# Performance work log

Measured on AMD Instinct MI355X. Metric: run time of the kernel, lower is better.

## Reference

```python
import jax, jax.numpy as jnp
import numpy as np

S = 1024      # sequence length
V = 32000     # vocab size
H = 1024      # hidden_dim
A = 128       # attn_size (module default)


def lstm_cell(x, h, c, Wih, Whh, b):
    # torch LSTM gate order: i, f, g, o
    g = x @ Wih.T + h @ Whh.T + b
    i, f, gg, o = jnp.split(g, 4)
    c = jax.nn.sigmoid(f) * c + jax.nn.sigmoid(i) * jnp.tanh(gg)
    h = jax.nn.sigmoid(o) * jnp.tanh(c)
    return h, c


def setup_inputs() -> dict:
    key = jax.random.key(0)
    ks = jax.random.split(key, 16)
    p = lambda k, shape: (jax.random.normal(k, shape, jnp.float32) * 0.02)
    return {
        'input_seq': jax.random.randint(ks[0], (S,), 0, V),
        'gold_seq': jax.random.randint(ks[1], (S,), 0, V),
        'embed': p(ks[2], (V, H)),
        'enc_Wih': p(ks[3], (4 * H, H)),
        'enc_Whh': p(ks[4], (4 * H, H)),
        'enc_b': jnp.zeros((4 * H,), jnp.float32),   # b_ih + b_hh combined
        'dec_Wih': p(ks[5], (4 * H, 2 * H)),          # decoder input = [prev, context]
        'dec_Whh': p(ks[6], (4 * H, H)),
        'dec_b': jnp.zeros((4 * H,), jnp.float32),
        'U_w': p(ks[7], (A, H)), 'U_b': jnp.zeros((A,), jnp.float32),
        'Wa_w': p(ks[8], (A, H)), 'Wa_b': jnp.zeros((A,), jnp.float32),
        'Va_w': p(ks[9], (1, A)), 'Va_b': jnp.zeros((1,), jnp.float32),
        'out_w': p(ks[10], (V, H)), 'out_b': jnp.zeros((V,), jnp.float32),
    }


def reference(input_seq, gold_seq, embed, enc_Wih, enc_Whh, enc_b,
              dec_Wih, dec_Whh, dec_b, U_w, U_b, Wa_w, Wa_b, Va_w, Va_b,
              out_w, out_b):
    Hd = embed.shape[1]
    x_emb = embed[input_seq]  # (S, H)

    def enc_step(carry, x):
        h, c = carry
        h, c = lstm_cell(x, h, c, enc_Wih, enc_Whh, enc_b)
        return (h, c), h

    zero = jnp.zeros((Hd,), x_emb.dtype)
    (h0, c0), enc_out = jax.lax.scan(enc_step, (zero, zero), x_emb)  # enc_out: (S, H)

    U_enc = enc_out @ U_w.T + U_b  # (S, A), hidden-independent part of additive attention

    # teacher forcing: prev_0 = zeros, prev_i = embed(gold[i-1]); relu applied each step
    prev = jnp.concatenate([jnp.zeros((1, Hd), x_emb.dtype), embed[gold_seq[:-1]]], axis=0)
    prev = jax.nn.relu(prev)  # (S, H)

    def dec_step(carry, p):
        h, c = carry
        # additive attention scores: V(tanh(U(enc) + W(h)))  -> (S, 1)
        scores = jnp.tanh(U_enc + h @ Wa_w.T + Wa_b) @ Va_w.T + Va_b
        # faithful to nn.Softmax() on a (S,1) tensor: torch picks dim=1 -> all ones
        w = jax.nn.softmax(scores, axis=1)  # (S, 1), == ones
        context = w[:, 0] @ enc_out         # (H,) == sum of encoder outputs
        x = jnp.concatenate([p, context])   # (2H,)
        h, c = lstm_cell(x, h, c, dec_Wih, dec_Whh, dec_b)
        logits = h @ out_w.T + out_b        # (V,)
        return (h, c), (logits, jnp.argmax(logits))

    _, (preds, idxs) = jax.lax.scan(dec_step, (h0, c0), prev)
    return preds, idxs  # (S, V) float logits, (S,) predicted ids
```

## Files before the change

### kernel.cpp

```cpp
#include <hip/hip_runtime.h>
#include <math.h>


#define S_LEN 1024
#define HDIM  1024
#define VDIM  32000

typedef float f4 __attribute__((ext_vector_type(4)));
typedef float f32x4 __attribute__((ext_vector_type(4)));
typedef short short8 __attribute__((ext_vector_type(8)));
typedef short sh4 __attribute__((ext_vector_type(4)));

__device__ __forceinline__ void agent_storef(float* p, float v) {
    __hip_atomic_store(p, v, __ATOMIC_RELAXED, __HIP_MEMORY_SCOPE_AGENT);
}
__device__ __forceinline__ float sigmoidf_(float x) {
    return 1.0f / (1.0f + expf(-x));
}
__device__ __forceinline__ void llc_load_4x4(const float* p, f4& a, f4& b,
                                             f4& c, f4& d) {
    asm volatile(
        "global_load_dwordx4 %0, %4, off sc0 sc1\n\t"
        "global_load_dwordx4 %1, %4, off offset:1024 sc0 sc1\n\t"
        "global_load_dwordx4 %2, %4, off offset:2048 sc0 sc1\n\t"
        "global_load_dwordx4 %3, %4, off offset:3072 sc0 sc1\n\t"
        "s_waitcnt vmcnt(0)"
        : "=&v"(a), "=&v"(b), "=&v"(c), "=&v"(d)
        : "v"(p) : "memory");
}
__device__ __forceinline__ bool any_nan16(f4 a, f4 b, f4 c, f4 d) {
    float s0 = (a.x + a.y) + (a.z + a.w);
    float s1 = (b.x + b.y) + (b.z + b.w);
    float s2 = (c.x + c.y) + (c.z + c.w);
    float s3 = (d.x + d.y) + (d.z + d.w);
    float s  = (s0 + s1) + (s2 + s3);
    return s != s;
}
__device__ __forceinline__ int swz(int s) {
    return (s & ~7) | ((s ^ (s >> 3)) & 7);
}
__device__ __forceinline__ void split_bf16(float x, unsigned short& h,
                                           unsigned short& l) {
    unsigned u = __float_as_uint(x);
    unsigned hr = (u + 0x7FFFu + ((u >> 16) & 1u)) >> 16;
    h = (unsigned short)hr;
    float hf = __uint_as_float(hr << 16);
    float r = x - hf;
    unsigned v = __float_as_uint(r);
    l = (unsigned short)((v + 0x7FFFu + ((v >> 16) & 1u)) >> 16);
}

template<int MODE>
__global__ __launch_bounds__(256)
void gemm_nt(const float* __restrict__ B, int ldb,
             const float* __restrict__ bias,
             float* __restrict__ C, int ldc,
             const float* __restrict__ embed,
             const int* __restrict__ gidx,
             int M, int N, int K)
{
    __shared__ float As[16][128];
    __shared__ float Bs[16][128];

    const int tid = threadIdx.x;
    const int m0 = blockIdx.y * 128;
    const int n0 = blockIdx.x * 128;

    float acc[8][8];
#pragma unroll
    for (int r = 0; r < 8; ++r)
#pragma unroll
        for (int c = 0; c < 8; ++c) acc[r][c] = 0.0f;

    const int ty = tid >> 4;
    const int tx = tid & 15;

    for (int k0 = 0; k0 < K; k0 += 16) {
#pragma unroll
        for (int q = 0; q < 2; ++q) {
            int id = tid * 2 + q;
            int m  = id >> 2;
            int c4 = (id & 3) * 4;
            float4 v;
            if (MODE == 1) {
                int row = gidx[m0 + m];
                v = *(const float4*)(embed + (size_t)row * HDIM + k0 + c4);
            } else {
                int mg = m0 + m;
                if (mg == 0) {
                    v = make_float4(0.f, 0.f, 0.f, 0.f);
                } else {
                    int row = gidx[mg - 1];
                    v = *(const float4*)(embed + (size_t)row * HDIM + k0 + c4);
                    v.x = fmaxf(v.x, 0.f); v.y = fmaxf(v.y, 0.f);
                    v.z = fmaxf(v.z, 0.f); v.w = fmaxf(v.w, 0.f);
                }
            }
            As[c4 + 0][m] = v.x; As[c4 + 1][m] = v.y;
            As[c4 + 2][m] = v.z; As[c4 + 3][m] = v.w;
        }
#pragma unroll
        for (int q = 0; q < 2; ++q) {
            int id = tid * 2 + q;
            int n  = id >> 2;
            int c4 = (id & 3) * 4;
            float4 v = *(const float4*)(B + (size_t)(n0 + n) * ldb + k0 + c4);
            Bs[c4 + 0][n] = v.x; Bs[c4 + 1][n] = v.y;
            Bs[c4 + 2][n] = v.z; Bs[c4 + 3][n] = v.w;
        }
        __syncthreads();

#pragma unroll
        for (int k = 0; k < 16; ++k) {
            float4 a0 = *(const float4*)&As[k][ty * 8];
            float4 a1 = *(const float4*)&As[k][ty * 8 + 4];
            float4 b0 = *(const float4*)&Bs[k][tx * 8];
            float4 b1 = *(const float4*)&Bs[k][tx * 8 + 4];
            float av[8] = {a0.x,a0.y,a0.z,a0.w,a1.x,a1.y,a1.z,a1.w};
            float bv[8] = {b0.x,b0.y,b0.z,b0.w,b1.x,b1.y,b1.z,b1.w};
#pragma unroll
            for (int r = 0; r < 8; ++r)
#pragma unroll
                for (int c = 0; c < 8; ++c)
                    acc[r][c] = fmaf(av[r], bv[c], acc[r][c]);
        }
        __syncthreads();
    }

    const int mbase = m0 + ty * 8;
    const int nbase = n0 + tx * 8;
#pragma unroll
    for (int r = 0; r < 8; ++r) {
        float4 o0, o1;
        o0.x = acc[r][0] + bias[nbase + 0];
        o0.y = acc[r][1] + bias[nbase + 1];
        o0.z = acc[r][2] + bias[nbase + 2];
        o0.w = acc[r][3] + bias[nbase + 3];
        o1.x = acc[r][4] + bias[nbase + 4];
        o1.y = acc[r][5] + bias[nbase + 5];
        o1.z = acc[r][6] + bias[nbase + 6];
        o1.w = acc[r][7] + bias[nbase + 7];
        *(float4*)(C + (size_t)(mbase + r) * ldc + nbase)     = o0;
        *(float4*)(C + (size_t)(mbase + r) * ldc + nbase + 4) = o1;
    }
}

__global__ __launch_bounds__(512, 2)
void lstm_seq(const float* __restrict__ Whh,
              const float* __restrict__ G,
              const float* __restrict__ h_init,
              const float* __restrict__ c_init,
              float* __restrict__ h_out,
              float* __restrict__ c_fin,
              float* __restrict__ csum_out,
              int slen)
{
    __shared__ f4 hbuf[256];
    const int tid = threadIdx.x;
    const int g   = blockIdx.x;
    const int wv  = tid >> 6;
    const int lg  = tid & 63;
    const int j   = g * 8 + wv;

    f4 W[4][4];
#pragma unroll
    for (int q = 0; q < 4; ++q)
#pragma unroll
        for (int i = 0; i < 4; ++i)
            W[q][i] = *(const f4*)(Whh + (size_t)(j + q * HDIM) * HDIM
                                   + 4 * lg + 256 * i);

    float c = 0.0f, csum = 0.0f;
    if (lg == 0) c = c_init[j];

    float gnow = G[(size_t)(lg & 3) * HDIM + j];

    for (int t = 0; t < slen; ++t) {
#pragma unroll
        for (int q = 0; q < 4; ++q)
#pragma unroll
            for (int i = 0; i < 4; ++i)
                asm volatile("" : "+v"(W[q][i]));

        const float* hp = (t == 0) ? h_init : (h_out + (size_t)(t - 1) * HDIM);

        if (wv == 0) {
            f4 a, b, cc, d;
            const float* p = hp + 4 * lg;
            for (;;) {
                llc_load_4x4(p, a, b, cc, d);
                if (!__any(any_nan16(a, b, cc, d))) break;
                __builtin_amdgcn_s_sleep(1);
            }
            hbuf[swz(lg)]       = a;
            hbuf[swz(64 + lg)]  = b;
            hbuf[swz(128 + lg)] = cc;
            hbuf[swz(192 + lg)] = d;
        }
        __syncthreads();

        int tn = (t + 1 < slen) ? (t + 1) : t;
        float gnext = G[(size_t)tn * (4 * HDIM) + (lg & 3) * HDIM + j];

        f4 h0 = hbuf[swz(lg)];
        f4 h1 = hbuf[swz(64 + lg)];
        f4 h2 = hbuf[swz(128 + lg)];
        f4 h3 = hbuf[swz(192 + lg)];
        float p0 = 0.f, p1 = 0.f, p2 = 0.f, p3 = 0.f;
        f4 hv;
#pragma unroll
        for (int i = 0; i < 4; ++i) {
            hv = (i == 0) ? h0 : (i == 1) ? h1 : (i == 2) ? h2 : h3;
            p0 = fmaf(W[0][i].x, hv.x, fmaf(W[0][i].y, hv.y,
                 fmaf(W[0][i].z, hv.z, fmaf(W[0][i].w, hv.w, p0))));
            p1 = fmaf(W[1][i].x, hv.x, fmaf(W[1][i].y, hv.y,
                 fmaf(W[1][i].z, hv.z, fmaf(W[1][i].w, hv.w, p1))));
            p2 = fmaf(W[2][i].x, hv.x, fmaf(W[2][i].y, hv.y,
                 fmaf(W[2][i].z, hv.z, fmaf(W[2][i].w, hv.w, p2))));
            p3 = fmaf(W[3][i].x, hv.x, fmaf(W[3][i].y, hv.y,
                 fmaf(W[3][i].z, hv.z, fmaf(W[3][i].w, hv.w, p3))));
        }

        float t01 = __shfl_xor((lg & 1) ? p0 : p1, 1);
        float s01 = ((lg & 1) ? p1 : p0) + t01;
        float t23 = __shfl_xor((lg & 1) ? p2 : p3, 1);
        float s23 = ((lg & 1) ? p3 : p2) + t23;
        float tq  = __shfl_xor((lg & 2) ? s01 : s23, 2);
        float s   = ((lg & 2) ? s23 : s01) + tq;
        s += __shfl_xor(s, 4);
        s += __shfl_xor(s, 8);
        s += __shfl_xor(s, 16);
        s += __shfl_xor(s, 32);

        float pre = s + gnow;
        float act = ((lg & 3) == 2) ? tanhf(pre) : sigmoidf_(pre);
        float a1 = __shfl(act, 1);
        float a2 = __shfl(act, 2);
        float a3 = __shfl(act, 3);

        if (lg == 0) {
            c = a1 * c + act * a2;
            float h = a3 * tanhf(c);
            csum += h;
            agent_storef(h_out + (size_t)t * HDIM + j, h);
        }
        gnow = gnext;
        __syncthreads();
    }

    if (lg == 0) {
        if (c_fin)    c_fin[j]    = c;
        if (csum_out) csum_out[j] = csum;
    }
}

__global__ __launch_bounds__(256)
void ctx_bias_k(const float* __restrict__ dec_Wih,
                const float* __restrict__ dec_b,
                const float* __restrict__ ctx,
                float* __restrict__ out)
{
    const int wv = threadIdx.x >> 6;
    const int lane = threadIdx.x & 63;
    const int r = blockIdx.x * 4 + wv;
    const float* wr = dec_Wih + (size_t)r * (2 * HDIM) + HDIM;
    float s = 0.f;
    for (int k = lane; k < HDIM; k += 64) s += wr[k] * ctx[k];
#pragma unroll
    for (int off = 32; off > 0; off >>= 1) s += __shfl_xor(s, off);
    if (lane == 0) out[r] = s + dec_b[r];
}

#define LSTR 40

__global__ __launch_bounds__(512, 1)
void logits_mfma(const float* __restrict__ Amat,
                 const float* __restrict__ Bmat,
                 const float* __restrict__ bias,
                 float* __restrict__ C,
                 unsigned long long* __restrict__ amax)
{
    __shared__ unsigned short Ah[256][LSTR], Al[256][LSTR];
    __shared__ unsigned short Bh[128][LSTR], Bl[128][LSTR];

    const int tid = threadIdx.x;
    const int l   = tid & 63;
    const int w   = tid >> 6;
    const int n0  = blockIdx.x * 128;
    const int m0  = blockIdx.y * 256;
    const int mb  = (w >> 1) * 64;
    const int nb  = (w & 1) * 64;

    f32x4 acc[4][4];
#pragma unroll
    for (int i = 0; i < 4; ++i)
#pragma unroll
        for (int jj = 0; jj < 4; ++jj) acc[i][jj] = (f32x4){0.f, 0.f, 0.f, 0.f};

    for (int k0 = 0; k0 < HDIM; k0 += 32) {
#pragma unroll
        for (int q = 0; q < 4; ++q) {
            int id  = q * 512 + tid;
            int row = id >> 3;
            int kq  = (id & 7) * 4;
            float4 av = *(const float4*)(Amat + (size_t)(m0 + row) * HDIM
                                         + k0 + kq);
            unsigned short h0,h1,h2,h3, l0,l1,l2,l3;
            split_bf16(av.x, h0, l0); split_bf16(av.y, h1, l1);
            split_bf16(av.z, h2, l2); split_bf16(av.w, h3, l3);
            sh4 hi = {(short)h0, (short)h1, (short)h2, (short)h3};
            sh4 lo = {(short)l0, (short)l1, (short)l2, (short)l3};
            *(sh4*)&Ah[row][kq] = hi;
            *(sh4*)&Al[row][kq] = lo;
        }
#pragma unroll
        for (int q = 0; q < 2; ++q) {
            int id  = q * 512 + tid;
            int row = id >> 3;
            int kq  = (id & 7) * 4;
            float4 bv = *(const float4*)(Bmat + (size_t)(n0 + row) * HDIM
                                         + k0 + kq);
            unsigned short h0,h1,h2,h3, l0,l1,l2,l3;
            split_bf16(bv.x, h0, l0); split_bf16(bv.y, h1, l1);
            split_bf16(bv.z, h2, l2); split_bf16(bv.w, h3, l3);
            sh4 hi = {(short)h0, (short)h1, (short)h2, (short)h3};
            sh4 lo = {(short)l0, (short)l1, (short)l2, (short)l3};
            *(sh4*)&Bh[row][kq] = hi;
            *(sh4*)&Bl[row][kq] = lo;
        }
        __syncthreads();

        const int kb = (l >> 4) * 8;
        short8 a_hi[4], a_lo[4], b_hi[4], b_lo[4];
#pragma unroll
        for (int i = 0; i < 4; ++i) {
            int ra = mb + i * 16 + (l & 15);
            int rb = nb + i * 16 + (l & 15);
            a_hi[i] = *(const short8*)&Ah[ra][kb];
            a_lo[i] = *(const short8*)&Al[ra][kb];
            b_hi[i] = *(const short8*)&Bh[rb][kb];
            b_lo[i] = *(const short8*)&Bl[rb][kb];
        }
#pragma unroll
        for (int i = 0; i < 4; ++i)
#pragma unroll
            for (int jj = 0; jj < 4; ++jj) {
                acc[i][jj] = __builtin_amdgcn_mfma_f32_16x16x32_bf16(
                    a_hi[i], b_hi[jj], acc[i][jj], 0, 0, 0);
                acc[i][jj] = __builtin_amdgcn_mfma_f32_16x16x32_bf16(
                    a_hi[i], b_lo[jj], acc[i][jj], 0, 0, 0);
                acc[i][jj] = __builtin_amdgcn_mfma_f32_16x16x32_bf16(
                    a_lo[i], b_hi[jj], acc[i][jj], 0, 0, 0);
            }
        __syncthreads();
    }

#pragma unroll
    for (int i = 0; i < 4; ++i) {
        const int mrow = m0 + mb + i * 16 + ((l >> 4) << 2);
        unsigned long long key[4] = {0ull, 0ull, 0ull, 0ull};
#pragma unroll
        for (int jj = 0; jj < 4; ++jj) {
            int n = n0 + nb + jj * 16 + (l & 15);
            float bv = bias[n];
            f32x4 o = acc[i][jj];
#pragma unroll
            for (int r = 0; r < 4; ++r) {
                float val = o[r] + bv;
                C[(size_t)(mrow + r) * VDIM + n] = val;
                unsigned um = __float_as_uint(val);
                um = (um & 0x80000000u) ? ~um : (um | 0x80000000u);
                unsigned long long k2 = ((unsigned long long)um << 32)
                    | (unsigned long long)(0xFFFFFFFFu - (unsigned)n);
                if (k2 > key[r]) key[r] = k2;
            }
        }
#pragma unroll
        for (int r = 0; r < 4; ++r) {
#pragma unroll
            for (int off = 1; off < 16; off <<= 1) {
                unsigned long long other = __shfl_xor(key[r], off);
                if (other > key[r]) key[r] = other;
            }
            if ((l & 15) == 0)
                atomicMax(&amax[mrow + r], key[r]);
        }
    }
}

__global__ __launch_bounds__(256)
void idx_final(const unsigned long long* __restrict__ amax,
               float* __restrict__ out_idx)
{
    int i = blockIdx.x * 256 + threadIdx.x;
    if (i < S_LEN) {
        unsigned col = 0xFFFFFFFFu - (unsigned)(amax[i] & 0xFFFFFFFFull);
        out_idx[i] = (float)col;
    }
}

extern "C" void kernel_launch(void* const* d_in, const int* in_sizes, int n_in,
                              void* d_out, int out_size, void* d_ws, size_t ws_size,
                              hipStream_t stream)
{
    (void)in_sizes; (void)n_in; (void)out_size; (void)ws_size;

    const int*   input_seq = (const int*)d_in[0];
    const int*   gold_seq  = (const int*)d_in[1];
    const float* embed     = (const float*)d_in[2];
    const float* enc_Wih   = (const float*)d_in[3];
    const float* enc_Whh   = (const float*)d_in[4];
    const float* enc_b     = (const float*)d_in[5];
    const float* dec_Wih   = (const float*)d_in[6];
    const float* dec_Whh   = (const float*)d_in[7];
    const float* dec_b     = (const float*)d_in[8];
    const float* out_w     = (const float*)d_in[15];
    const float* out_b     = (const float*)d_in[16];

    float* out = (float*)d_out;
    float* G_enc = out;
    float* G_dec = out + 4194304;

    char* wsb = (char*)d_ws;
    unsigned long long* amax = (unsigned long long*)wsb;
    float* zerovec = (float*)(wsb + 8192);
    float* c0      = zerovec + 1024;
    float* ctx     = c0 + 1024;
    float* ctxb    = ctx + 1024;
    float* enc_out = ctxb + 4096;
    float* dec_h   = enc_out + 1048576;

    hipMemsetAsync(d_ws, 0, 12288, stream);
    hipMemsetAsync(enc_out, 0xFF, (size_t)S_LEN * HDIM * 4, stream);
    hipMemsetAsync(dec_h,   0xFF, (size_t)S_LEN * HDIM * 4, stream);

    gemm_nt<1><<<dim3(32, 8), 256, 0, stream>>>(
        enc_Wih, HDIM, enc_b, G_enc, 4 * HDIM,
        embed, input_seq, S_LEN, 4 * HDIM, HDIM);

    lstm_seq<<<128, 512, 0, stream>>>(
        enc_Whh, G_enc, zerovec, zerovec, enc_out, c0, ctx, S_LEN);

    ctx_bias_k<<<1024, 256, 0, stream>>>(dec_Wih, dec_b, ctx, ctxb);

    gemm_nt<2><<<dim3(32, 8), 256, 0, stream>>>(
        dec_Wih, 2 * HDIM, ctxb, G_dec, 4 * HDIM,
        embed, gold_seq, S_LEN, 4 * HDIM, HDIM);

    lstm_seq<<<128, 512, 0, stream>>>(
        dec_Whh, G_dec, enc_out + (size_t)(S_LEN - 1) * HDIM, c0,
        dec_h, nullptr, nullptr, S_LEN);

    logits_mfma<<<dim3(VDIM / 128, S_LEN / 256), 512, 0, stream>>>(
        dec_h, out_w, out_b, out, amax);

    idx_final<<<4, 256, 0, stream>>>(amax, out + (size_t)S_LEN * VDIM);
}
```

Before: 4.715 ms.

## Use split-bf16 MFMA for gate projection GEMMs and double-buffer LSTM h broadcast

Replaces the scalar FP32 tiled GEMM for the encoder and decoder input-gate projections with an MFMA kernel. It splits fp32 operands into hi/lo bf16 parts and accumulates three products to keep near-fp32 accuracy. The LSTM recurrence kernel also double-buffers its shared h buffer by timestep parity, which lets it drop the trailing per-step __syncthreads. The GEMMs are a small share of runtime next to the two sequential 1024-step LSTMs. Removing the barrier could shave latency from every recurrent step, but only if the parity buffers are truly race-free.

Result: faster. 4.372 ms (-7.3%).

```diff
diff --git a/kernel.cpp b/kernel.cpp
--- a/kernel.cpp
+++ b/kernel.cpp
@@ -50,98 +50,121 @@
     l = (unsigned short)((v + 0x7FFFu + ((v >> 16) & 1u)) >> 16);
 }
 
+#define LSTR 40
+
 template<int MODE>
-__global__ __launch_bounds__(256)
-void gemm_nt(const float* __restrict__ B, int ldb,
-             const float* __restrict__ bias,
-             float* __restrict__ C, int ldc,
-             const float* __restrict__ embed,
-             const int* __restrict__ gidx,
-             int M, int N, int K)
-{
-    __shared__ float As[16][128];
-    __shared__ float Bs[16][128];
+__global__ __launch_bounds__(512, 1)
+void g_mfma(const float* __restrict__ B, int ldb,
+            const float* __restrict__ bias,
+            float* __restrict__ C, int ldc,
+            const float* __restrict__ embed,
+            const int* __restrict__ gidx)
+{
+    __shared__ unsigned short Ah[256][LSTR], Al[256][LSTR];
+    __shared__ unsigned short Bh[128][LSTR], Bl[128][LSTR];
 
     const int tid = threadIdx.x;
-    const int m0 = blockIdx.y * 128;
-    const int n0 = blockIdx.x * 128;
-
-    float acc[8][8];
-#pragma unroll
-    for (int r = 0; r < 8; ++r)
-#pragma unroll
-        for (int c = 0; c < 8; ++c) acc[r][c] = 0.0f;
-
-    const int ty = tid >> 4;
-    const int tx = tid & 15;
-
-    for (int k0 = 0; k0 < K; k0 += 16) {
+    const int l   = tid & 63;
+    const int w   = tid >> 6;
+    const int n0  = blockIdx.x * 128;
+    const int m0  = blockIdx.y * 256;
+    const int mb  = (w >> 1) * 64;
+    const int nb  = (w & 1) * 64;
+
+    int  arow[4];
+    bool azero[4];
+#pragma unroll
+    for (int q = 0; q < 4; ++q) {
+        int row = (q * 512 + tid) >> 3;
+        int m = m0 + row;
+        if (MODE == 1) { arow[q] = gidx[m]; azero[q] = false; }
+        else { azero[q] = (m == 0); arow[q] = azero[q] ? 0 : gidx[m - 1]; }
+    }
+
+    f32x4 acc[4][4];
+#pragma unroll
+    for (int i = 0; i < 4; ++i)
+#pragma unroll
+        for (int jj = 0; jj < 4; ++jj) acc[i][jj] = (f32x4){0.f, 0.f, 0.f, 0.f};
+
+    for (int k0 = 0; k0 < HDIM; k0 += 32) {
+#pragma unroll
+        for (int q = 0; q < 4; ++q) {
+            int id  = q * 512 + tid;
+            int row = id >> 3;
+            int kq  = (id & 7) * 4;
+            float4 av;
+            if (MODE == 2 && azero[q]) {
+                av = make_float4(0.f, 0.f, 0.f, 0.f);
+            } else {
+                av = *(const float4*)(embed + (size_t)arow[q] * HDIM + k0 + kq);
+                if (MODE == 2) {
+                    av.x = fmaxf(av.x, 0.f); av.y = fmaxf(av.y, 0.f);
+                    av.z = fmaxf(av.z, 0.f); av.w = fmaxf(av.w, 0.f);
+                }
+            }
+            unsigned short h0,h1,h2,h3, l0,l1,l2,l3;
+            split_bf16(av.x, h0, l0); split_bf16(av.y, h1, l1);
+            split_bf16(av.z, h2, l2); split_bf16(av.w, h3, l3);
+            sh4 hi = {(short)h0, (short)h1, (short)h2, (short)h3};
+            sh4 lo = {(short)l0, (short)l1, (short)l2, (short)l3};
+            *(sh4*)&Ah[row][kq] = hi;
+            *(sh4*)&Al[row][kq] = lo;
+        }
 #pragma unroll
         for (int q = 0; q < 2; ++q) {
-            int id = tid * 2 + q;
-            int m  = id >> 2;
-            int c4 = (id & 3) * 4;
-            float4 v;
-            if (MODE == 1) {
-                int row = gidx[m0 + m];
-                v = *(const float4*)(embed + (size_t)row * HDIM + k0 + c4);
-            } else {
-                int mg = m0 + m;
-                if (mg == 0) {
-                    v = make_float4(0.f, 0.f, 0.f, 0.f);
-                } else {
-                    int row = gidx[mg - 1];
-                    v = *(const float4*)(embed + (size_t)row * HDIM + k0 + c4);
-                    v.x = fmaxf(v.x, 0.f); v.y = fmaxf(v.y, 0.f);
-                    v.z = fmaxf(v.z, 0.f); v.w = fmaxf(v.w, 0.f);
-                }
-            }
-            As[c4 + 0][m] = v.x; As[c4 + 1][m] = v.y;
-            As[c4 + 2][m] = v.z; As[c4 + 3][m] = v.w;
-        }
-#pragma unroll
-        for (int q = 0; q < 2; ++q) {
-            int id = tid * 2 + q;
-            int n  = id >> 2;
-            int c4 = (id & 3) * 4;
-            float4 v = *(const float4*)(B + (size_t)(n0 + n) * ldb + k0 + c4);
-            Bs[c4 + 0][n] = v.x; Bs[c4 + 1][n] = v.y;
-            Bs[c4 + 2][n] = v.z; Bs[c4 + 3][n] = v.w;
+            int id  = q * 512 + tid;
+            int row = id >> 3;
+            int kq  = (id & 7) * 4;
+            float4 bv = *(const float4*)(B + (size_t)(n0 + row) * ldb
+                                         + k0 + kq);
+            unsigned short h0,h1,h2,h3, l0,l1,l2,l3;
+            split_bf16(bv.x, h0, l0); split_bf16(bv.y, h1, l1);
+            split_bf16(bv.z, h2, l2); split_bf16(bv.w, h3, l3);
+            sh4 hi = {(short)h0, (short)h1, (short)h2, (short)h3};
+            sh4 lo = {(short)l0, (short)l1, (short)l2, (short)l3};
+            *(sh4*)&Bh[row][kq] = hi;
+            *(sh4*)&Bl[row][kq] = lo;
         }
         __syncthreads();
 
-#pragma unroll
-        for (int k = 0; k < 16; ++k) {
-            float4 a0 = *(const float4*)&As[k][ty * 8];
-            float4 a1 = *(const float4*)&As[k][ty * 8 + 4];
-            float4 b0 = *(const float4*)&Bs[k][tx * 8];
-            float4 b1 = *(const float4*)&Bs[k][tx * 8 + 4];
-            float av[8] = {a0.x,a0.y,a0.z,a0.w,a1.x,a1.y,a1.z,a1.w};
-            float bv[8] = {b0.x,b0.y,b0.z,b0.w,b1.x,b1.y,b1.z,b1.w};
-#pragma unroll
-            for (int r = 0; r < 8; ++r)
-#pragma unroll
-                for (int c = 0; c < 8; ++c)
-                    acc[r][c] = fmaf(av[r], bv[c], acc[r][c]);
-        }
+        const int kb = (l >> 4) * 8;
+        short8 a_hi[4], a_lo[4], b_hi[4], b_lo[4];
+#pragma unroll
+        for (int i = 0; i < 4; ++i) {
+            int ra = mb + i * 16 + (l & 15);
+            int rb = nb + i * 16 + (l & 15);
+            a_hi[i] = *(const short8*)&Ah[ra][kb];
+            a_lo[i] = *(const short8*)&Al[ra][kb];
+            b_hi[i] = *(const short8*)&Bh[rb][kb];
+            b_lo[i] = *(const short8*)&Bl[rb][kb];
+        }
+#pragma unroll
+        for (int i = 0; i < 4; ++i)
+#pragma unroll
+            for (int jj = 0; jj < 4; ++jj) {
+                acc[i][jj] = __builtin_amdgcn_mfma_f32_16x16x32_bf16(
+                    a_hi[i], b_hi[jj], acc[i][jj], 0, 0, 0);
+                acc[i][jj] = __builtin_amdgcn_mfma_f32_16x16x32_bf16(
+                    a_hi[i], b_lo[jj], acc[i][jj], 0, 0, 0);
+                acc[i][jj] = __builtin_amdgcn_mfma_f32_16x16x32_bf16(
+                    a_lo[i], b_hi[jj], acc[i][jj], 0, 0, 0);
+            }
         __syncthreads();
     }
 
-    const int mbase = m0 + ty * 8;
-    const int nbase = n0 + tx * 8;
-#pragma unroll
-    for (int r = 0; r < 8; ++r) {
-        float4 o0, o1;
-        o0.x = acc[r][0] + bias[nbase + 0];
-        o0.y = acc[r][1] + bias[nbase + 1];
-        o0.z = acc[r][2] + bias[nbase + 2];
-        o0.w = acc[r][3] + bias[nbase + 3];
-        o1.x = acc[r][4] + bias[nbase + 4];
-        o1.y = acc[r][5] + bias[nbase + 5];
-        o1.z = acc[r][6] + bias[nbase + 6];
-        o1.w = acc[r][7] + bias[nbase + 7];
-        *(float4*)(C + (size_t)(mbase + r) * ldc + nbase)     = o0;
-        *(float4*)(C + (size_t)(mbase + r) * ldc + nbase + 4) = o1;
+#pragma unroll
+    for (int i = 0; i < 4; ++i) {
+        const int mrow = m0 + mb + i * 16 + ((l >> 4) << 2);
+#pragma unroll
+        for (int jj = 0; jj < 4; ++jj) {
+            int n = n0 + nb + jj * 16 + (l & 15);
+            float bv = bias[n];
+            f32x4 o = acc[i][jj];
+#pragma unroll
+            for (int r = 0; r < 4; ++r)
+                C[(size_t)(mrow + r) * ldc + n] = o[r] + bv;
+        }
     }
 }
 
@@ -155,7 +178,7 @@
               float* __restrict__ csum_out,
               int slen)
 {
-    __shared__ f4 hbuf[256];
+    __shared__ f4 hbuf[2][256];
     const int tid = threadIdx.x;
     const int g   = blockIdx.x;
     const int wv  = tid >> 6;
@@ -183,6 +206,7 @@
                 asm volatile("" : "+v"(W[q][i]));
 
         const float* hp = (t == 0) ? h_init : (h_out + (size_t)(t - 1) * HDIM);
+        f4* hb = hbuf[t & 1];
 
         if (wv == 0) {
             f4 a, b, cc, d;
@@ -192,20 +216,20 @@
                 if (!__any(any_nan16(a, b, cc, d))) break;
                 __builtin_amdgcn_s_sleep(1);
             }
-            hbuf[swz(lg)]       = a;
-            hbuf[swz(64 + lg)]  = b;
-            hbuf[swz(128 + lg)] = cc;
-            hbuf[swz(192 + lg)] = d;
+            hb[swz(lg)]       = a;
+            hb[swz(64 + lg)]  = b;
+            hb[swz(128 + lg)] = cc;
+            hb[swz(192 + lg)] = d;
         }
         __syncthreads();
 
         int tn = (t + 1 < slen) ? (t + 1) : t;
         float gnext = G[(size_t)tn * (4 * HDIM) + (lg & 3) * HDIM + j];
 
-        f4 h0 = hbuf[swz(lg)];
-        f4 h1 = hbuf[swz(64 + lg)];
-        f4 h2 = hbuf[swz(128 + lg)];
-        f4 h3 = hbuf[swz(192 + lg)];
+        f4 h0 = hb[swz(lg)];
+        f4 h1 = hb[swz(64 + lg)];
+        f4 h2 = hb[swz(128 + lg)];
+        f4 h3 = hb[swz(192 + lg)];
         float p0 = 0.f, p1 = 0.f, p2 = 0.f, p3 = 0.f;
         f4 hv;
 #pragma unroll
@@ -245,7 +269,6 @@
             agent_storef(h_out + (size_t)t * HDIM + j, h);
         }
         gnow = gnext;
-        __syncthreads();
     }
 
     if (lg == 0) {
@@ -270,8 +293,6 @@
     for (int off = 32; off > 0; off >>= 1) s += __shfl_xor(s, off);
     if (lane == 0) out[r] = s + dec_b[r];
 }
-
-#define LSTR 40
 
 __global__ __launch_bounds__(512, 1)
 void logits_mfma(const float* __restrict__ Amat,
@@ -434,18 +455,16 @@
     hipMemsetAsync(enc_out, 0xFF, (size_t)S_LEN * HDIM * 4, stream);
     hipMemsetAsync(dec_h,   0xFF, (size_t)S_LEN * HDIM * 4, stream);
 
-    gemm_nt<1><<<dim3(32, 8), 256, 0, stream>>>(
-        enc_Wih, HDIM, enc_b, G_enc, 4 * HDIM,
-        embed, input_seq, S_LEN, 4 * HDIM, HDIM);
+    g_mfma<1><<<dim3(32, 4), 512, 0, stream>>>(
+        enc_Wih, HDIM, enc_b, G_enc, 4 * HDIM, embed, input_seq);
 
     lstm_seq<<<128, 512, 0, stream>>>(
         enc_Whh, G_enc, zerovec, zerovec, enc_out, c0, ctx, S_LEN);
 
     ctx_bias_k<<<1024, 256, 0, stream>>>(dec_Wih, dec_b, ctx, ctxb);
 
-    gemm_nt<2><<<dim3(32, 8), 256, 0, stream>>>(
-        dec_Wih, 2 * HDIM, ctxb, G_dec, 4 * HDIM,
-        embed, gold_seq, S_LEN, 4 * HDIM, HDIM);
+    g_mfma<2><<<dim3(32, 4), 512, 0, stream>>>(
+        dec_Wih, 2 * HDIM, ctxb, G_dec, 4 * HDIM, embed, gold_seq);
 
     lstm_seq<<<128, 512, 0, stream>>>(
         dec_Whh, G_dec, enc_out + (size_t)(S_LEN - 1) * HDIM, c0,
```
